# Kernel tuning notes

Measured on AMD Instinct MI355X. Metric: run time of the kernel, lower is better.

## Reference

```python
import jax, jax.numpy as jnp
import numpy as np

LN_EPS = 1e-5  # ParlAI LAYER_NORM_EPS
B, S, D, H, E, V = 4, 512, 512, 2048, 8, 32000


def setup_inputs() -> dict:
    key = jax.random.key(0)
    ks = jax.random.split(key, 6)
    x = jax.random.normal(ks[0], (B, S, D), dtype=jnp.float32)
    orig_input = jax.random.randint(ks[1], (B, S), 0, V)          # token ids
    hash_bin_map = jax.random.randint(ks[2], (V,), 0, E, dtype=jnp.int32)
    W1 = jax.random.normal(ks[3], (E, D, H), dtype=jnp.float32) * 0.02
    b1 = jnp.zeros((E, H), dtype=jnp.float32)
    W2 = jax.random.normal(ks[4], (E, H, D), dtype=jnp.float32) * 0.02
    b2 = jnp.zeros((E, D), dtype=jnp.float32)
    gamma = jnp.ones((D,), dtype=jnp.float32)
    beta = jnp.zeros((D,), dtype=jnp.float32)
    return {"x": x, "W1": W1, "b1": b1, "W2": W2, "b2": b2,
            "gamma": gamma, "beta": beta,
            "orig_input": orig_input, "hash_bin_map": hash_bin_map}


def _layernorm(z, gamma, beta):
    mu = jnp.mean(z, axis=-1, keepdims=True)
    var = jnp.var(z, axis=-1, keepdims=True)
    return (z - mu) * jax.lax.rsqrt(var + LN_EPS) * gamma + beta


def reference(x, W1, b1, W2, b2, gamma, beta, orig_input, hash_bin_map):
    # per-token expert assignment via hash of token id
    bins = hash_bin_map[orig_input]                    # [B, S] int
    n_experts = W1.shape[0]
    ffn_out = jnp.zeros_like(x)
    # loop over the small fixed expert set; mask-combine replaces gather/scatter
    for e in range(n_experts):
        h = jax.nn.relu(jnp.einsum('bsd,dh->bsh', x, W1[e]) + b1[e])
        y = jnp.einsum('bsh,hd->bsd', h, W2[e]) + b2[e]
        ffn_out = ffn_out + jnp.where((bins == e)[..., None], y, 0.0)
    # residual + shared LayerNorm (every token belongs to exactly one bin)
    return _layernorm(x + ffn_out, gamma, beta)
```

## Files before the change

### kernel.cpp

```cpp
#include <hip/hip_runtime.h>
#include <hip/hip_bf16.h>
#include <stdint.h>

#define D_DIM 512
#define H_DIM 2048
#define E_NUM 8
#define TM 64
#define CAP 2560
#define MAXRT 6

typedef __attribute__((ext_vector_type(8))) short short8;
typedef __attribute__((ext_vector_type(4))) float floatx4;

union Pack4 { short4 u; __hip_bfloat16 h[4]; };

__global__ __launch_bounds__(256) void bin_kernel(
    const int* __restrict__ orig, const int* __restrict__ hmap,
    int* __restrict__ gidx, int* __restrict__ meta, int ntok)
{
    __shared__ int cnt[E_NUM];
    __shared__ int cur[E_NUM];
    int tid = threadIdx.x;
    int lane = tid & 63;
    if (tid < E_NUM) cnt[tid] = 0;
    __syncthreads();

    int nIter = (ntok + 255) >> 8;
    for (int it = 0; it < nIter; it++) {
        int t = it * 256 + tid;
        int b = (t < ntok) ? hmap[orig[t]] : -1;
#pragma unroll
        for (int e2 = 0; e2 < E_NUM; e2++) {
            unsigned long long m = __ballot(b == e2);
            if (lane == 0) {
                int c = (int)__popcll(m);
                if (c) atomicAdd(&cnt[e2], c);
            }
        }
    }
    __syncthreads();
    if (tid == 0) {
        int off = 0;
        for (int e = 0; e < E_NUM; e++) {
            int ne = cnt[e];
            int nt = (ne + TM - 1) / TM;
            meta[e] = off; meta[8 + e] = ne; meta[16 + e] = nt;
            cur[e] = off;
            off += nt * TM;
        }
        meta[24] = off;
    }
    __syncthreads();
    for (int it = 0; it < nIter; it++) {
        int t = it * 256 + tid;
        int b = (t < ntok) ? hmap[orig[t]] : -1;
        int pos = 0;
#pragma unroll
        for (int e2 = 0; e2 < E_NUM; e2++) {
            unsigned long long m = __ballot(b == e2);
            int base = 0;
            if (lane == 0) {
                int c = (int)__popcll(m);
                if (c) base = atomicAdd(&cur[e2], c);
            }
            base = __shfl(base, 0, 64);
            if (b == e2)
                pos = base + (int)__popcll(m & ((1ull << lane) - 1));
        }
        if (b >= 0) gidx[pos] = t;
    }
}

__global__ __launch_bounds__(128) void gather_kernel(
    const float* __restrict__ x, const int* __restrict__ gidx,
    const int* __restrict__ meta, __hip_bfloat16* __restrict__ Xg)
{
    int g = blockIdx.x;
    int e = -1, local = 0;
#pragma unroll
    for (int i = 0; i < E_NUM; i++) {
        int p = meta[i], nt = meta[16 + i];
        if (g >= p && g < p + nt * TM) { e = i; local = g - p; }
    }
    if (e < 0) return;
    int tid = threadIdx.x;
    __hip_bfloat16* orow = Xg + (size_t)g * D_DIM + tid * 4;
    if (local < meta[8 + e]) {
        int t = gidx[g];
        float4 v = ((const float4*)(x + (size_t)t * D_DIM))[tid];
        orow[0] = __float2bfloat16(v.x);
        orow[1] = __float2bfloat16(v.y);
        orow[2] = __float2bfloat16(v.z);
        orow[3] = __float2bfloat16(v.w);
    } else {
        orow[0] = __float2bfloat16(0.f);
        orow[1] = __float2bfloat16(0.f);
        orow[2] = __float2bfloat16(0.f);
        orow[3] = __float2bfloat16(0.f);
    }
}

template <int WN, int ASTRIDE, int KTOT, int KS, bool RELU>
__global__ __launch_bounds__(256) void moe_gemm_kernel(
    const __hip_bfloat16* __restrict__ A,
    const float* __restrict__ W,
    const float* __restrict__ bias,
    __hip_bfloat16* __restrict__ OutBf,
    __hip_bfloat16* __restrict__ OutP,
    const int* __restrict__ meta)
{
    constexpr int KLEN = KTOT / KS;
    constexpr int NI = KLEN / 64;
    constexpr int AJ = MAXRT * 64 * 8 / 256;
    const int e = blockIdx.x;
    const int n0 = blockIdx.z * 64;
    const int ks = blockIdx.y;
    const int kbase = ks * KLEN;

    int nt = meta[16 + e];
    if (nt > MAXRT) nt = MAXRT;
    const int row0 = meta[e];
    const int rows8 = nt * 64 * 8;

    __shared__ __align__(16) __hip_bfloat16 As[384 * 64];
    __shared__ __align__(16) __hip_bfloat16 Bs[64 * 64];

    const int tid = threadIdx.x;
    const int lane = tid & 63, w = tid >> 6;
    const int quad = lane >> 4, l16 = lane & 15;
    const int kq = tid >> 4;
    const int nb = tid & 15;

    const __hip_bfloat16* Ab = A + (size_t)row0 * ASTRIDE + kbase;
    const float* Wb = W + ((size_t)e * KTOT + kbase) * WN + n0;

    floatx4 acc[MAXRT][4] = {};
    short8 ar[AJ];
    float4 br[4];

#define LOADA(k0) do {                                                        \
    _Pragma("unroll")                                                         \
    for (int j = 0; j < AJ; j++) {                                            \
        int c = tid + j * 256;                                                \
        if (c < rows8) {                                                      \
            int row = c >> 3;                                                 \
            int kk = ((c & 7) * 16) ^ ((row & 7) * 16);            \
            ar[j] = *(const short8*)(Ab + (size_t)row * ASTRIDE + (k0) + (kk >> 1)); \
        }                                                                     \
    }                                                                         \
} while (0)

#define WRITEA() do {                                                         \
    _Pragma("unroll")                                                         \
    for (int j = 0; j < AJ; j++) {                                            \
        int c = tid + j * 256;                                                \
        if (c < rows8)                                                        \
            *(short8*)((char*)As + c * 16) = ar[j];                           \
    }                                                                         \
} while (0)

#define LOADB(k0) do {                                                        \
    _Pragma("unroll")                                                         \
    for (int r = 0; r < 4; r++)                                               \
        br[r] = *(const float4*)(Wb + (size_t)((k0) + kq * 4 + r) * WN + nb * 4); \
} while (0)

#define WRITEB() do {                                                         \
    _Pragma("unroll")                                                         \
    for (int j = 0; j < 4; j++) {                                             \
        int n = nb * 4 + j;                                                   \
        Pack4 pk;                                                             \
        _Pragma("unroll")                                                     \
        for (int r = 0; r < 4; r++)                                           \
            pk.h[r] = __float2bfloat16(reinterpret_cast<const float*>(&br[r])[j]); \
        *(short4*)((char*)Bs + n * 128 + ((kq * 8) ^ (((n >> 2) & 7) * 16))) = pk.u; \
    }                                                                         \
} while (0)

    LOADA(0);
    LOADB(0);

    for (int i = 0; i < NI; i++) {
        __syncthreads();
        WRITEA();
        WRITEB();
        __syncthreads();
        if (i + 1 < NI) {
            LOADA((i + 1) * 64);
            LOADB((i + 1) * 64);
        }
#pragma unroll
        for (int kf = 0; kf < 2; kf++) {
            int kb = kf * 64 + quad * 16;
            short8 b[4];
#pragma unroll
            for (int ni = 0; ni < 4; ni++) {
                int n = ni * 16 + l16;
                b[ni] = *(const short8*)((char*)Bs + n * 128 + (kb ^ (((n >> 2) & 7) * 16)));
            }
#pragma unroll
            for (int si = 0; si < MAXRT; si++) {
                if (si < nt) {
                    int row = (w + 4 * si) * 16 + l16;
                    short8 a = *(const short8*)((char*)As + row * 128 + (kb ^ ((row & 7) * 16)));
#pragma unroll
                    for (int ni = 0; ni < 4; ni++)
                        acc[si][ni] = __builtin_amdgcn_mfma_f32_16x16x32_bf16(
                            a, b[ni], acc[si][ni], 0, 0, 0);
                }
            }
        }
    }

#pragma unroll
    for (int si = 0; si < MAXRT; si++) {
        if (si >= nt) break;
        int s = w + 4 * si;
#pragma unroll
        for (int ni = 0; ni < 4; ni++) {
            int col = n0 + ni * 16 + l16;
            float bv = RELU ? bias[e * WN + col] : 0.f;
#pragma unroll
            for (int r = 0; r < 4; r++) {
                int grow = row0 + s * 16 + quad * 4 + r;
                float v = acc[si][ni][r] + bv;
                if constexpr (RELU) {
                    v = v > 0.f ? v : 0.f;
                    OutBf[(size_t)grow * WN + col] = __float2bfloat16(v);
                } else {
                    OutP[((size_t)ks * CAP + grow) * WN + col] = __float2bfloat16(v);
                }
            }
        }
    }
#undef LOADA
#undef WRITEA
#undef LOADB
#undef WRITEB
}

__global__ __launch_bounds__(128) void ln_kernel(
    const float* __restrict__ x, const __hip_bfloat16* __restrict__ Yp,
    const float* __restrict__ b2,
    const float* __restrict__ gamma, const float* __restrict__ beta,
    const int* __restrict__ gidx, const int* __restrict__ meta,
    float* __restrict__ out)
{
    int g = blockIdx.x;
    int e = -1;
#pragma unroll
    for (int i = 0; i < E_NUM; i++) {
        int p = meta[i], ne = meta[8 + i];
        if (g >= p && g - p < ne) e = i;
    }
    if (e < 0) return;
    int t = gidx[g];
    int tid = threadIdx.x;

    float4 xv = ((const float4*)(x + (size_t)t * D_DIM))[tid];
    float4 bb = ((const float4*)(b2 + (size_t)e * D_DIM))[tid];
    float z0 = xv.x + bb.x, z1 = xv.y + bb.y, z2 = xv.z + bb.z, z3 = xv.w + bb.w;
#pragma unroll
    for (int s4 = 0; s4 < 4; s4++) {
        union { short4 u; __hip_bfloat16 h[4]; } yv;
        yv.u = ((const short4*)(Yp + (size_t)(s4 * CAP + g) * D_DIM))[tid];
        z0 += __bfloat162float(yv.h[0]);
        z1 += __bfloat162float(yv.h[1]);
        z2 += __bfloat162float(yv.h[2]);
        z3 += __bfloat162float(yv.h[3]);
    }

    float s = z0 + z1 + z2 + z3;
    float ss = z0 * z0 + z1 * z1 + z2 * z2 + z3 * z3;
#pragma unroll
    for (int off = 32; off > 0; off >>= 1) {
        s  += __shfl_down(s, off, 64);
        ss += __shfl_down(ss, off, 64);
    }
    __shared__ float red[4];
    int lane = tid & 63, wv = tid >> 6;
    if (lane == 0) { red[wv] = s; red[2 + wv] = ss; }
    __syncthreads();
    float S = red[0] + red[1];
    float SS = red[2] + red[3];
    float mu = S * (1.f / D_DIM);
    float var = SS * (1.f / D_DIM) - mu * mu;
    float inv = rsqrtf(var + 1e-5f);

    float4 gv = ((const float4*)gamma)[tid];
    float4 bv = ((const float4*)beta)[tid];
    float4 o;
    o.x = (z0 - mu) * inv * gv.x + bv.x;
    o.y = (z1 - mu) * inv * gv.y + bv.y;
    o.z = (z2 - mu) * inv * gv.z + bv.z;
    o.w = (z3 - mu) * inv * gv.w + bv.w;
    ((float4*)(out + (size_t)t * D_DIM))[tid] = o;
}

extern "C" void kernel_launch(void* const* d_in, const int* in_sizes, int n_in,
                              void* d_out, int out_size, void* d_ws, size_t ws_size,
                              hipStream_t stream)
{
    const float* x     = (const float*)d_in[0];
    const float* W1    = (const float*)d_in[1];
    const float* b1    = (const float*)d_in[2];
    const float* W2    = (const float*)d_in[3];
    const float* b2    = (const float*)d_in[4];
    const float* gamma = (const float*)d_in[5];
    const float* beta  = (const float*)d_in[6];
    const int* orig    = (const int*)d_in[7];
    const int* hmap    = (const int*)d_in[8];
    float* out = (float*)d_out;
    int ntok = in_sizes[7];

    char* ws = (char*)d_ws;
    __hip_bfloat16* Yp  = (__hip_bfloat16*)(ws);
    __hip_bfloat16* Hb  = (__hip_bfloat16*)(ws + 10485760);
    __hip_bfloat16* Xg  = (__hip_bfloat16*)(ws + 20971520);
    int*            gidx= (int*)(ws + 23592960);
    int*            meta= (int*)(ws + 23603200);

    hipLaunchKernelGGL(bin_kernel, dim3(1), dim3(256), 0, stream,
                       orig, hmap, gidx, meta, ntok);
    hipLaunchKernelGGL(gather_kernel, dim3(CAP), dim3(128), 0, stream,
                       x, gidx, meta, Xg);
    hipLaunchKernelGGL((moe_gemm_kernel<H_DIM, D_DIM, D_DIM, 1, true>),
                       dim3(E_NUM, 1, H_DIM / 64), dim3(256), 0, stream,
                       Xg, W1, b1, Hb, (__hip_bfloat16*)nullptr, meta);
    hipLaunchKernelGGL((moe_gemm_kernel<D_DIM, H_DIM, H_DIM, 4, false>),
                       dim3(E_NUM, 4, D_DIM / 64), dim3(256), 0, stream,
                       Hb, W2, (const float*)nullptr, (__hip_bfloat16*)nullptr, Yp, meta);
    hipLaunchKernelGGL(ln_kernel, dim3(CAP), dim3(128), 0, stream,
                       x, Yp, b2, gamma, beta, gidx, meta, out);
}
```

Measured before the change: 160.5 us.

## Split MoE GEMM blocks per 64-row tile instead of whole expert

Each GEMM block now handles a single 64-row tile of one expert's tokens, selected by blockIdx.y, rather than looping over up to six row tiles per block. Blocks beyond an expert's tile count exit early. Warps are laid out 2x2 over a 64x64 output tile, so shared A storage shrinks and accumulator registers drop. Launch bounds request 4 blocks per CU to raise occupancy. In exchange, each W tile is reloaded and converted from fp32 once per row tile instead of once per expert, which multiplies weight traffic.

New measurement: 169.8 us. 5.8% more time.

```diff
diff --git a/kernel.cpp b/kernel.cpp
--- a/kernel.cpp
+++ b/kernel.cpp
@@ -101,7 +101,7 @@
 }
 
 template <int WN, int ASTRIDE, int KTOT, int KS, bool RELU>
-__global__ __launch_bounds__(256) void moe_gemm_kernel(
+__global__ __launch_bounds__(256, 4) void moe_gemm_kernel(
     const __hip_bfloat16* __restrict__ A,
     const float* __restrict__ W,
     const float* __restrict__ bias,
@@ -111,52 +111,46 @@
 {
     constexpr int KLEN = KTOT / KS;
     constexpr int NI = KLEN / 64;
-    constexpr int AJ = MAXRT * 64 * 8 / 256;
     const int e = blockIdx.x;
+    const int rt = blockIdx.y % MAXRT;
+    const int ks = blockIdx.y / MAXRT;
     const int n0 = blockIdx.z * 64;
-    const int ks = blockIdx.y;
     const int kbase = ks * KLEN;
 
-    int nt = meta[16 + e];
-    if (nt > MAXRT) nt = MAXRT;
-    const int row0 = meta[e];
-    const int rows8 = nt * 64 * 8;
-
-    __shared__ __align__(16) __hip_bfloat16 As[384 * 64];
+    const int nt = meta[16 + e];
+    if (rt >= nt) return;
+    const int row0 = meta[e] + rt * 64;
+
+    __shared__ __align__(16) __hip_bfloat16 As[64 * 64];
     __shared__ __align__(16) __hip_bfloat16 Bs[64 * 64];
 
     const int tid = threadIdx.x;
     const int lane = tid & 63, w = tid >> 6;
     const int quad = lane >> 4, l16 = lane & 15;
+    const int wr = w >> 1, wc = w & 1;
     const int kq = tid >> 4;
     const int nb = tid & 15;
 
+    const int c0 = tid, c1 = tid + 256;
+    const int arow0 = c0 >> 3, arow1 = c1 >> 3;
+    const int akk0 = ((c0 & 7) * 16) ^ ((arow0 & 7) * 16);
+    const int akk1 = ((c1 & 7) * 16) ^ ((arow1 & 7) * 16);
+
     const __hip_bfloat16* Ab = A + (size_t)row0 * ASTRIDE + kbase;
     const float* Wb = W + ((size_t)e * KTOT + kbase) * WN + n0;
 
-    floatx4 acc[MAXRT][4] = {};
-    short8 ar[AJ];
+    floatx4 acc[2][2] = {};
+    short8 ar[2];
     float4 br[4];
 
 #define LOADA(k0) do {                                                        \
-    _Pragma("unroll")                                                         \
-    for (int j = 0; j < AJ; j++) {                                            \
-        int c = tid + j * 256;                                                \
-        if (c < rows8) {                                                      \
-            int row = c >> 3;                                                 \
-            int kk = ((c & 7) * 16) ^ ((row & 7) * 16);            \
-            ar[j] = *(const short8*)(Ab + (size_t)row * ASTRIDE + (k0) + (kk >> 1)); \
-        }                                                                     \
-    }                                                                         \
+    ar[0] = *(const short8*)(Ab + (size_t)arow0 * ASTRIDE + (k0) + (akk0 >> 1)); \
+    ar[1] = *(const short8*)(Ab + (size_t)arow1 * ASTRIDE + (k0) + (akk1 >> 1)); \
 } while (0)
 
 #define WRITEA() do {                                                         \
-    _Pragma("unroll")                                                         \
-    for (int j = 0; j < AJ; j++) {                                            \
-        int c = tid + j * 256;                                                \
-        if (c < rows8)                                                        \
-            *(short8*)((char*)As + c * 16) = ar[j];                           \
-    }                                                                         \
+    *(short8*)((char*)As + c0 * 16) = ar[0];                                  \
+    *(short8*)((char*)As + c1 * 16) = ar[1];                                  \
 } while (0)
 
 #define LOADB(k0) do {                                                        \
@@ -192,38 +186,36 @@
 #pragma unroll
         for (int kf = 0; kf < 2; kf++) {
             int kb = kf * 64 + quad * 16;
-            short8 b[4];
-#pragma unroll
-            for (int ni = 0; ni < 4; ni++) {
-                int n = ni * 16 + l16;
+            short8 a[2], b[2];
+#pragma unroll
+            for (int mi = 0; mi < 2; mi++) {
+                int row = wr * 32 + mi * 16 + l16;
+                a[mi] = *(const short8*)((char*)As + row * 128 + (kb ^ ((row & 7) * 16)));
+            }
+#pragma unroll
+            for (int ni = 0; ni < 2; ni++) {
+                int n = wc * 32 + ni * 16 + l16;
                 b[ni] = *(const short8*)((char*)Bs + n * 128 + (kb ^ (((n >> 2) & 7) * 16)));
             }
 #pragma unroll
-            for (int si = 0; si < MAXRT; si++) {
-                if (si < nt) {
-                    int row = (w + 4 * si) * 16 + l16;
-                    short8 a = *(const short8*)((char*)As + row * 128 + (kb ^ ((row & 7) * 16)));
-#pragma unroll
-                    for (int ni = 0; ni < 4; ni++)
-                        acc[si][ni] = __builtin_amdgcn_mfma_f32_16x16x32_bf16(
-                            a, b[ni], acc[si][ni], 0, 0, 0);
-                }
-            }
-        }
-    }
-
-#pragma unroll
-    for (int si = 0; si < MAXRT; si++) {
-        if (si >= nt) break;
-        int s = w + 4 * si;
-#pragma unroll
-        for (int ni = 0; ni < 4; ni++) {
-            int col = n0 + ni * 16 + l16;
-            float bv = RELU ? bias[e * WN + col] : 0.f;
+            for (int mi = 0; mi < 2; mi++)
+#pragma unroll
+                for (int ni = 0; ni < 2; ni++)
+                    acc[mi][ni] = __builtin_amdgcn_mfma_f32_16x16x32_bf16(
+                        a[mi], b[ni], acc[mi][ni], 0, 0, 0);
+        }
+    }
+
+#pragma unroll
+    for (int ni = 0; ni < 2; ni++) {
+        int col = n0 + wc * 32 + ni * 16 + l16;
+        float bv = RELU ? bias[e * WN + col] : 0.f;
+#pragma unroll
+        for (int mi = 0; mi < 2; mi++) {
 #pragma unroll
             for (int r = 0; r < 4; r++) {
-                int grow = row0 + s * 16 + quad * 4 + r;
-                float v = acc[si][ni][r] + bv;
+                int grow = row0 + wr * 32 + mi * 16 + quad * 4 + r;
+                float v = acc[mi][ni][r] + bv;
                 if constexpr (RELU) {
                     v = v > 0.f ? v : 0.f;
                     OutBf[(size_t)grow * WN + col] = __float2bfloat16(v);
@@ -325,10 +317,10 @@
     hipLaunchKernelGGL(gather_kernel, dim3(CAP), dim3(128), 0, stream,
                        x, gidx, meta, Xg);
     hipLaunchKernelGGL((moe_gemm_kernel<H_DIM, D_DIM, D_DIM, 1, true>),
-                       dim3(E_NUM, 1, H_DIM / 64), dim3(256), 0, stream,
+                       dim3(E_NUM, MAXRT, H_DIM / 64), dim3(256), 0, stream,
                        Xg, W1, b1, Hb, (__hip_bfloat16*)nullptr, meta);
     hipLaunchKernelGGL((moe_gemm_kernel<D_DIM, H_DIM, H_DIM, 4, false>),
-                       dim3(E_NUM, 4, D_DIM / 64), dim3(256), 0, stream,
+                       dim3(E_NUM, MAXRT * 4, D_DIM / 64), dim3(256), 0, stream,
                        Hb, W2, (const float*)nullptr, (__hip_bfloat16*)nullptr, Yp, meta);
     hipLaunchKernelGGL(ln_kernel, dim3(CAP), dim3(128), 0, stream,
                        x, Yp, b2, gamma, beta, gidx, meta, out);
```

## Use 2x2 warp tiling, double-buffer register prefetch, and reorder grid in MoE GEMM

Applied to the files above, without the earlier changes.

Each wave's tile changes from one 16-row strip across all 64 columns to a 32x32 sub-tile per 64-row tile, which raises reuse of A fragments per B fragment loaded from LDS. Global prefetch now holds two register stages (ar0/ar1, br0/br1), with the loop unrolled by two so that loads for k+2 are in flight during compute. The grid is reordered so that expert index is the slowest dimension. This costs extra registers that may reduce occupancy, and the loop assumes NI is even (true for 8 and 8).

After: 164.0 us. 1.02x slower.

```diff
diff --git a/kernel.cpp b/kernel.cpp
--- a/kernel.cpp
+++ b/kernel.cpp
@@ -112,8 +112,8 @@
     constexpr int KLEN = KTOT / KS;
     constexpr int NI = KLEN / 64;
     constexpr int AJ = MAXRT * 64 * 8 / 256;
-    const int e = blockIdx.x;
-    const int n0 = blockIdx.z * 64;
+    const int e = blockIdx.z;
+    const int n0 = blockIdx.x * 64;
     const int ks = blockIdx.y;
     const int kbase = ks * KLEN;
 
@@ -128,107 +128,131 @@
     const int tid = threadIdx.x;
     const int lane = tid & 63, w = tid >> 6;
     const int quad = lane >> 4, l16 = lane & 15;
+    const int wr = w >> 1, wc = w & 1;
     const int kq = tid >> 4;
     const int nb = tid & 15;
 
     const __hip_bfloat16* Ab = A + (size_t)row0 * ASTRIDE + kbase;
     const float* Wb = W + ((size_t)e * KTOT + kbase) * WN + n0;
 
-    floatx4 acc[MAXRT][4] = {};
-    short8 ar[AJ];
-    float4 br[4];
-
-#define LOADA(k0) do {                                                        \
+    floatx4 acc[MAXRT][2][2] = {};
+    short8 ar0[AJ], ar1[AJ];
+    float4 br0[4], br1[4];
+
+#define LOADA(dst, k0) do {                                                   \
     _Pragma("unroll")                                                         \
     for (int j = 0; j < AJ; j++) {                                            \
         int c = tid + j * 256;                                                \
         if (c < rows8) {                                                      \
             int row = c >> 3;                                                 \
             int kk = ((c & 7) * 16) ^ ((row & 7) * 16);            \
-            ar[j] = *(const short8*)(Ab + (size_t)row * ASTRIDE + (k0) + (kk >> 1)); \
+            dst[j] = *(const short8*)(Ab + (size_t)row * ASTRIDE + (k0) + (kk >> 1)); \
         }                                                                     \
     }                                                                         \
 } while (0)
 
-#define WRITEA() do {                                                         \
+#define WRITEA(src) do {                                                      \
     _Pragma("unroll")                                                         \
     for (int j = 0; j < AJ; j++) {                                            \
         int c = tid + j * 256;                                                \
         if (c < rows8)                                                        \
-            *(short8*)((char*)As + c * 16) = ar[j];                           \
+            *(short8*)((char*)As + c * 16) = src[j];                          \
     }                                                                         \
 } while (0)
 
-#define LOADB(k0) do {                                                        \
+#define LOADB(dst, k0) do {                                                   \
     _Pragma("unroll")                                                         \
     for (int r = 0; r < 4; r++)                                               \
-        br[r] = *(const float4*)(Wb + (size_t)((k0) + kq * 4 + r) * WN + nb * 4); \
-} while (0)
-
-#define WRITEB() do {                                                         \
+        dst[r] = *(const float4*)(Wb + (size_t)((k0) + kq * 4 + r) * WN + nb * 4); \
+} while (0)
+
+#define WRITEB(src) do {                                                      \
     _Pragma("unroll")                                                         \
     for (int j = 0; j < 4; j++) {                                             \
         int n = nb * 4 + j;                                                   \
         Pack4 pk;                                                             \
         _Pragma("unroll")                                                     \
         for (int r = 0; r < 4; r++)                                           \
-            pk.h[r] = __float2bfloat16(reinterpret_cast<const float*>(&br[r])[j]); \
+            pk.h[r] = __float2bfloat16(reinterpret_cast<const float*>(&src[r])[j]); \
         *(short4*)((char*)Bs + n * 128 + ((kq * 8) ^ (((n >> 2) & 7) * 16))) = pk.u; \
     }                                                                         \
 } while (0)
 
-    LOADA(0);
-    LOADB(0);
-
-    for (int i = 0; i < NI; i++) {
+#define COMPUTE() do {                                                        \
+    _Pragma("unroll")                                                         \
+    for (int kf = 0; kf < 2; kf++) {                                          \
+        int kb = kf * 64 + quad * 16;                                         \
+        short8 b[2];                                                          \
+        _Pragma("unroll")                                                     \
+        for (int ni = 0; ni < 2; ni++) {                                      \
+            int n = wc * 32 + ni * 16 + l16;                                  \
+            b[ni] = *(const short8*)((char*)Bs + n * 128 + (kb ^ (((n >> 2) & 7) * 16))); \
+        }                                                                     \
+        _Pragma("unroll")                                                     \
+        for (int rt = 0; rt < MAXRT; rt++) {                                  \
+            if (rt < nt) {                                                    \
+                short8 a[2];                                                  \
+                _Pragma("unroll")                                             \
+                for (int mi = 0; mi < 2; mi++) {                              \
+                    int row = rt * 64 + wr * 32 + mi * 16 + l16;              \
+                    a[mi] = *(const short8*)((char*)As + row * 128 + (kb ^ ((row & 7) * 16))); \
+                }                                                             \
+                _Pragma("unroll")                                             \
+                for (int mi = 0; mi < 2; mi++)                                \
+                    _Pragma("unroll")                                         \
+                    for (int ni = 0; ni < 2; ni++)                            \
+                        acc[rt][mi][ni] = __builtin_amdgcn_mfma_f32_16x16x32_bf16( \
+                            a[mi], b[ni], acc[rt][mi][ni], 0, 0, 0);          \
+            }                                                                 \
+        }                                                                     \
+    }                                                                         \
+} while (0)
+
+    LOADA(ar0, 0);
+    LOADB(br0, 0);
+    LOADA(ar1, 64);
+    LOADB(br1, 64);
+
+    for (int i = 0; i < NI; i += 2) {
         __syncthreads();
-        WRITEA();
-        WRITEB();
+        WRITEA(ar0);
+        WRITEB(br0);
         __syncthreads();
-        if (i + 1 < NI) {
-            LOADA((i + 1) * 64);
-            LOADB((i + 1) * 64);
-        }
-#pragma unroll
-        for (int kf = 0; kf < 2; kf++) {
-            int kb = kf * 64 + quad * 16;
-            short8 b[4];
-#pragma unroll
-            for (int ni = 0; ni < 4; ni++) {
-                int n = ni * 16 + l16;
-                b[ni] = *(const short8*)((char*)Bs + n * 128 + (kb ^ (((n >> 2) & 7) * 16)));
-            }
-#pragma unroll
-            for (int si = 0; si < MAXRT; si++) {
-                if (si < nt) {
-                    int row = (w + 4 * si) * 16 + l16;
-                    short8 a = *(const short8*)((char*)As + row * 128 + (kb ^ ((row & 7) * 16)));
-#pragma unroll
-                    for (int ni = 0; ni < 4; ni++)
-                        acc[si][ni] = __builtin_amdgcn_mfma_f32_16x16x32_bf16(
-                            a, b[ni], acc[si][ni], 0, 0, 0);
-                }
-            }
-        }
-    }
-
-#pragma unroll
-    for (int si = 0; si < MAXRT; si++) {
-        if (si >= nt) break;
-        int s = w + 4 * si;
-#pragma unroll
-        for (int ni = 0; ni < 4; ni++) {
-            int col = n0 + ni * 16 + l16;
+        if (i + 2 < NI) {
+            LOADA(ar0, (i + 2) * 64);
+            LOADB(br0, (i + 2) * 64);
+        }
+        COMPUTE();
+        __syncthreads();
+        WRITEA(ar1);
+        WRITEB(br1);
+        __syncthreads();
+        if (i + 3 < NI) {
+            LOADA(ar1, (i + 3) * 64);
+            LOADB(br1, (i + 3) * 64);
+        }
+        COMPUTE();
+    }
+
+#pragma unroll
+    for (int rt = 0; rt < MAXRT; rt++) {
+        if (rt >= nt) break;
+#pragma unroll
+        for (int ni = 0; ni < 2; ni++) {
+            int col = n0 + wc * 32 + ni * 16 + l16;
             float bv = RELU ? bias[e * WN + col] : 0.f;
 #pragma unroll
-            for (int r = 0; r < 4; r++) {
-                int grow = row0 + s * 16 + quad * 4 + r;
-                float v = acc[si][ni][r] + bv;
-                if constexpr (RELU) {
-                    v = v > 0.f ? v : 0.f;
-                    OutBf[(size_t)grow * WN + col] = __float2bfloat16(v);
-                } else {
-                    OutP[((size_t)ks * CAP + grow) * WN + col] = __float2bfloat16(v);
+            for (int mi = 0; mi < 2; mi++) {
+#pragma unroll
+                for (int r = 0; r < 4; r++) {
+                    int grow = row0 + rt * 64 + wr * 32 + mi * 16 + quad * 4 + r;
+                    float v = acc[rt][mi][ni][r] + bv;
+                    if constexpr (RELU) {
+                        v = v > 0.f ? v : 0.f;
+                        OutBf[(size_t)grow * WN + col] = __float2bfloat16(v);
+                    } else {
+                        OutP[((size_t)ks * CAP + grow) * WN + col] = __float2bfloat16(v);
+                    }
                 }
             }
         }
@@ -237,6 +261,7 @@
 #undef WRITEA
 #undef LOADB
 #undef WRITEB
+#undef COMPUTE
 }
 
 __global__ __launch_bounds__(128) void ln_kernel(
@@ -325,10 +350,10 @@
     hipLaunchKernelGGL(gather_kernel, dim3(CAP), dim3(128), 0, stream,
                        x, gidx, meta, Xg);
     hipLaunchKernelGGL((moe_gemm_kernel<H_DIM, D_DIM, D_DIM, 1, true>),
-                       dim3(E_NUM, 1, H_DIM / 64), dim3(256), 0, stream,
+                       dim3(H_DIM / 64, 1, E_NUM), dim3(256), 0, stream,
                        Xg, W1, b1, Hb, (__hip_bfloat16*)nullptr, meta);
     hipLaunchKernelGGL((moe_gemm_kernel<D_DIM, H_DIM, H_DIM, 4, false>),
-                       dim3(E_NUM, 4, D_DIM / 64), dim3(256), 0, stream,
+                       dim3(D_DIM / 64, 4, E_NUM), dim3(256), 0, stream,
                        Hb, W2, (const float*)nullptr, (__hip_bfloat16*)nullptr, Yp, meta);
     hipLaunchKernelGGL(ln_kernel, dim3(CAP), dim3(128), 0, stream,
                        x, Yp, b2, gamma, beta, gidx, meta, out);
```

## Use 2x2 warp tiling in MoE GEMM, reorder grid, simplify binning

Applied to the files above, without the earlier changes.

The GEMM warp layout changes from each wave owning a 16-row strip across all 64 columns to a 2x2 arrangement. Each wave now covers 32x32 per row tile, which cuts the B-fragment LDS reads per wave and improves fragment reuse. The grid is reordered so the N-tile index is fastest and the expert index is slowest, so consecutive blocks share the same expert weights. The bin kernel drops the ballot/popcount aggregation for plain per-token shared atomics, which adds atomic contention in that small single-block kernel.

Measured after the change: 152.7 us. 1.05x faster.

```diff
diff --git a/kernel.cpp b/kernel.cpp
--- a/kernel.cpp
+++ b/kernel.cpp
@@ -21,22 +21,11 @@
     __shared__ int cnt[E_NUM];
     __shared__ int cur[E_NUM];
     int tid = threadIdx.x;
-    int lane = tid & 63;
     if (tid < E_NUM) cnt[tid] = 0;
     __syncthreads();
-
-    int nIter = (ntok + 255) >> 8;
-    for (int it = 0; it < nIter; it++) {
-        int t = it * 256 + tid;
-        int b = (t < ntok) ? hmap[orig[t]] : -1;
-#pragma unroll
-        for (int e2 = 0; e2 < E_NUM; e2++) {
-            unsigned long long m = __ballot(b == e2);
-            if (lane == 0) {
-                int c = (int)__popcll(m);
-                if (c) atomicAdd(&cnt[e2], c);
-            }
-        }
+    for (int t = tid; t < ntok; t += 256) {
+        int b = hmap[orig[t]];
+        atomicAdd(&cnt[b], 1);
     }
     __syncthreads();
     if (tid == 0) {
@@ -51,23 +40,10 @@
         meta[24] = off;
     }
     __syncthreads();
-    for (int it = 0; it < nIter; it++) {
-        int t = it * 256 + tid;
-        int b = (t < ntok) ? hmap[orig[t]] : -1;
-        int pos = 0;
-#pragma unroll
-        for (int e2 = 0; e2 < E_NUM; e2++) {
-            unsigned long long m = __ballot(b == e2);
-            int base = 0;
-            if (lane == 0) {
-                int c = (int)__popcll(m);
-                if (c) base = atomicAdd(&cur[e2], c);
-            }
-            base = __shfl(base, 0, 64);
-            if (b == e2)
-                pos = base + (int)__popcll(m & ((1ull << lane) - 1));
-        }
-        if (b >= 0) gidx[pos] = t;
+    for (int t = tid; t < ntok; t += 256) {
+        int b = hmap[orig[t]];
+        int p = atomicAdd(&cur[b], 1);
+        gidx[p] = t;
     }
 }
 
@@ -112,8 +88,8 @@
     constexpr int KLEN = KTOT / KS;
     constexpr int NI = KLEN / 64;
     constexpr int AJ = MAXRT * 64 * 8 / 256;
-    const int e = blockIdx.x;
-    const int n0 = blockIdx.z * 64;
+    const int e = blockIdx.z;
+    const int n0 = blockIdx.x * 64;
     const int ks = blockIdx.y;
     const int kbase = ks * KLEN;
 
@@ -128,13 +104,14 @@
     const int tid = threadIdx.x;
     const int lane = tid & 63, w = tid >> 6;
     const int quad = lane >> 4, l16 = lane & 15;
+    const int wr = w >> 1, wc = w & 1;
     const int kq = tid >> 4;
     const int nb = tid & 15;
 
     const __hip_bfloat16* Ab = A + (size_t)row0 * ASTRIDE + kbase;
     const float* Wb = W + ((size_t)e * KTOT + kbase) * WN + n0;
 
-    floatx4 acc[MAXRT][4] = {};
+    floatx4 acc[MAXRT][2][2] = {};
     short8 ar[AJ];
     float4 br[4];
 
@@ -192,43 +169,51 @@
 #pragma unroll
         for (int kf = 0; kf < 2; kf++) {
             int kb = kf * 64 + quad * 16;
-            short8 b[4];
-#pragma unroll
-            for (int ni = 0; ni < 4; ni++) {
-                int n = ni * 16 + l16;
+            short8 b[2];
+#pragma unroll
+            for (int ni = 0; ni < 2; ni++) {
+                int n = wc * 32 + ni * 16 + l16;
                 b[ni] = *(const short8*)((char*)Bs + n * 128 + (kb ^ (((n >> 2) & 7) * 16)));
             }
 #pragma unroll
-            for (int si = 0; si < MAXRT; si++) {
-                if (si < nt) {
-                    int row = (w + 4 * si) * 16 + l16;
-                    short8 a = *(const short8*)((char*)As + row * 128 + (kb ^ ((row & 7) * 16)));
-#pragma unroll
-                    for (int ni = 0; ni < 4; ni++)
-                        acc[si][ni] = __builtin_amdgcn_mfma_f32_16x16x32_bf16(
-                            a, b[ni], acc[si][ni], 0, 0, 0);
+            for (int rt = 0; rt < MAXRT; rt++) {
+                if (rt < nt) {
+                    short8 a[2];
+#pragma unroll
+                    for (int mi = 0; mi < 2; mi++) {
+                        int row = rt * 64 + wr * 32 + mi * 16 + l16;
+                        a[mi] = *(const short8*)((char*)As + row * 128 + (kb ^ ((row & 7) * 16)));
+                    }
+#pragma unroll
+                    for (int mi = 0; mi < 2; mi++)
+#pragma unroll
+                        for (int ni = 0; ni < 2; ni++)
+                            acc[rt][mi][ni] = __builtin_amdgcn_mfma_f32_16x16x32_bf16(
+                                a[mi], b[ni], acc[rt][mi][ni], 0, 0, 0);
                 }
             }
         }
     }
 
 #pragma unroll
-    for (int si = 0; si < MAXRT; si++) {
-        if (si >= nt) break;
-        int s = w + 4 * si;
-#pragma unroll
-        for (int ni = 0; ni < 4; ni++) {
-            int col = n0 + ni * 16 + l16;
+    for (int rt = 0; rt < MAXRT; rt++) {
+        if (rt >= nt) break;
+#pragma unroll
+        for (int ni = 0; ni < 2; ni++) {
+            int col = n0 + wc * 32 + ni * 16 + l16;
             float bv = RELU ? bias[e * WN + col] : 0.f;
 #pragma unroll
-            for (int r = 0; r < 4; r++) {
-                int grow = row0 + s * 16 + quad * 4 + r;
-                float v = acc[si][ni][r] + bv;
-                if constexpr (RELU) {
-                    v = v > 0.f ? v : 0.f;
-                    OutBf[(size_t)grow * WN + col] = __float2bfloat16(v);
-                } else {
-                    OutP[((size_t)ks * CAP + grow) * WN + col] = __float2bfloat16(v);
+            for (int mi = 0; mi < 2; mi++) {
+#pragma unroll
+                for (int r = 0; r < 4; r++) {
+                    int grow = row0 + rt * 64 + wr * 32 + mi * 16 + quad * 4 + r;
+                    float v = acc[rt][mi][ni][r] + bv;
+                    if constexpr (RELU) {
+                        v = v > 0.f ? v : 0.f;
+                        OutBf[(size_t)grow * WN + col] = __float2bfloat16(v);
+                    } else {
+                        OutP[((size_t)ks * CAP + grow) * WN + col] = __float2bfloat16(v);
+                    }
                 }
             }
         }
@@ -325,10 +310,10 @@
     hipLaunchKernelGGL(gather_kernel, dim3(CAP), dim3(128), 0, stream,
                        x, gidx, meta, Xg);
     hipLaunchKernelGGL((moe_gemm_kernel<H_DIM, D_DIM, D_DIM, 1, true>),
-                       dim3(E_NUM, 1, H_DIM / 64), dim3(256), 0, stream,
+                       dim3(H_DIM / 64, 1, E_NUM), dim3(256), 0, stream,
                        Xg, W1, b1, Hb, (__hip_bfloat16*)nullptr, meta);
     hipLaunchKernelGGL((moe_gemm_kernel<D_DIM, H_DIM, H_DIM, 4, false>),
-                       dim3(E_NUM, 4, D_DIM / 64), dim3(256), 0, stream,
+                       dim3(D_DIM / 64, 4, E_NUM), dim3(256), 0, stream,
                        Hb, W2, (const float*)nullptr, (__hip_bfloat16*)nullptr, Yp, meta);
     hipLaunchKernelGGL(ln_kernel, dim3(CAP), dim3(128), 0, stream,
                        x, Yp, b2, gamma, beta, gidx, meta, out);
```
